# Optimization experiments

Hardware: AMD Instinct MI355X
Metric: run time of the kernel (lower is better)

Reference implementation:

```python
import jax, jax.numpy as jnp
import numpy as np

B, MAX_POINTS = 4, 100000
NPX, NPY, C = 512, 512, 64


def setup_inputs() -> dict:
    key = jax.random.key(0)
    k1, k2, k3, k4, k5, k6, k7 = jax.random.split(key, 7)
    grid_flow_embeddings = jax.random.normal(k1, (B, C, NPX, NPY), dtype=jnp.float32)
    point_cloud = jax.random.normal(k2, (B, MAX_POINTS, C), dtype=jnp.float32)
    # same pillar index replicated across the channel dim, as produced upstream
    pillar_idx = jax.random.randint(k3, (B, MAX_POINTS, 1), 0, NPX * NPY)
    indices = jnp.broadcast_to(pillar_idx, (B, MAX_POINTS, C)).astype(jnp.int64)
    # Linear(128, 32) and Linear(32, 3), torch layout: W [out, in], b [out]
    Y_w = jax.random.normal(k4, (32, 128), dtype=jnp.float32) / np.sqrt(128.0)
    Y_b = jax.random.normal(k5, (32,), dtype=jnp.float32) * 0.01
    Z_w = jax.random.normal(k6, (3, 32), dtype=jnp.float32) / np.sqrt(32.0)
    Z_b = jax.random.normal(k7, (3,), dtype=jnp.float32) * 0.01
    return {
        "grid_flow_embeddings": grid_flow_embeddings,
        "point_cloud": point_cloud,
        "indices": indices,
        "Y_w": Y_w,
        "Y_b": Y_b,
        "Z_w": Z_w,
        "Z_b": Z_b,
    }


def reference(grid_flow_embeddings, point_cloud, indices, Y_w, Y_b, Z_w, Z_b):
    b, c, nx, ny = grid_flow_embeddings.shape
    # permute (B,C,X,Y) -> (B,X,Y,C), flatten -> (B, X*Y, C)
    grid_flat = jnp.transpose(grid_flow_embeddings, (0, 2, 3, 1)).reshape(b, nx * ny, c)
    # gather along dim 1 with per-element indices (B, P, C)
    cell_embeddings = jnp.take_along_axis(grid_flat, indices, axis=1)
    full = jnp.concatenate([cell_embeddings, point_cloud], axis=2)  # (B, P, 128)
    full = jnp.einsum("bpf,of->bpo", full, Y_w) + Y_b                # (B, P, 32)
    full = jnp.einsum("bpf,of->bpo", full, Z_w) + Z_b                # (B, P, 3)
    return full
```

## Files before the change

### kernel.cpp

```cpp
#include <hip/hip_runtime.h>

#define BATCH 4
#define PTS   100000
#define CH    64
#define NPIX  (512 * 512)


#define WS_AG    0
#define WS_AP    1024
#define WS_BIAS  2048
#define WS_G3    4096

__global__ __launch_bounds__(128) void fold_weights_kernel(
    const float* __restrict__ Yw,
    const float* __restrict__ Yb,
    const float* __restrict__ Zw,
    const float* __restrict__ Zb,
    float* __restrict__ ws)
{
    const int f = threadIdx.x;
    float a0 = 0.f, a1 = 0.f, a2 = 0.f;
    for (int k = 0; k < 32; ++k) {
        const float y = Yw[k * 128 + f];
        a0 += Zw[0 * 32 + k] * y;
        a1 += Zw[1 * 32 + k] * y;
        a2 += Zw[2 * 32 + k] * y;
    }
    float4* dst = (f < 64) ? (float4*)((char*)ws + WS_AG) + f
                           : (float4*)((char*)ws + WS_AP) + (f - 64);
    *dst = make_float4(a0, a1, a2, 0.f);

    if (f == 0) {
        float b0 = Zb[0], b1 = Zb[1], b2 = Zb[2];
        for (int k = 0; k < 32; ++k) {
            const float y = Yb[k];
            b0 += Zw[0 * 32 + k] * y;
            b1 += Zw[1 * 32 + k] * y;
            b2 += Zw[2 * 32 + k] * y;
        }
        *(float4*)((char*)ws + WS_BIAS) = make_float4(b0, b1, b2, 0.f);
    }
}

__global__ __launch_bounds__(256) void grid_reduce_kernel(
    const float* __restrict__ grid,
    const float* __restrict__ ws_in,
    float* __restrict__ ws_out)
{
    __shared__ float4 sAg[64];
    if (threadIdx.x < 64)
        sAg[threadIdx.x] = ((const float4*)((const char*)ws_in + WS_AG))[threadIdx.x];
    __syncthreads();

    const int b = blockIdx.x >> 8;
    const int grp = ((blockIdx.x & 255) << 8) | threadIdx.x;
    const size_t pix0 = (size_t)grp * 4;

    const float* gbase = grid + (size_t)b * CH * NPIX + pix0;

    float4 acc0 = make_float4(0.f, 0.f, 0.f, 0.f);
    float4 acc1 = acc0;
    float4 acc2 = acc0;
#pragma unroll 8
    for (int c = 0; c < 64; ++c) {
        const float4 g = *(const float4*)(gbase + (size_t)c * NPIX);
        const float4 a = sAg[c];
        acc0.x += g.x * a.x; acc0.y += g.y * a.x; acc0.z += g.z * a.x; acc0.w += g.w * a.x;
        acc1.x += g.x * a.y; acc1.y += g.y * a.y; acc1.z += g.z * a.y; acc1.w += g.w * a.y;
        acc2.x += g.x * a.z; acc2.y += g.y * a.z; acc2.z += g.z * a.z; acc2.w += g.w * a.z;
    }

    float4* out4 = (float4*)((char*)ws_out + WS_G3) + ((size_t)b * NPIX + pix0);
    out4[0] = make_float4(acc0.x, acc1.x, acc2.x, 0.f);
    out4[1] = make_float4(acc0.y, acc1.y, acc2.y, 0.f);
    out4[2] = make_float4(acc0.z, acc1.z, acc2.z, 0.f);
    out4[3] = make_float4(acc0.w, acc1.w, acc2.w, 0.f);
}

__global__ __launch_bounds__(256) void point_kernel(
    const float* __restrict__ pc,
    const int*   __restrict__ idx,
    const float* __restrict__ ws,
    float* __restrict__ out)
{
    __shared__ float4 sAp[64];
    __shared__ float4 sBias;
    if (threadIdx.x < 64)
        sAp[threadIdx.x] = ((const float4*)((const char*)ws + WS_AP))[threadIdx.x];
    if (threadIdx.x == 64)
        sBias = *(const float4*)((const char*)ws + WS_BIAS);
    __syncthreads();

    const long long g = (long long)blockIdx.x * 256 + threadIdx.x;
    if (g >= (long long)BATCH * PTS) return;
    const int b = (int)(g / PTS);
    const int p = (int)(g % PTS);

    const int pillar = idx[((long long)b * PTS + p) * CH];
    const float4 gcell = ((const float4*)((const char*)ws + WS_G3))[(size_t)b * NPIX + pillar];

    float z0 = gcell.x + sBias.x;
    float z1 = gcell.y + sBias.y;
    float z2 = gcell.z + sBias.z;

    const float4* pb = (const float4*)(pc + ((size_t)b * PTS + p) * CH);
#pragma unroll
    for (int c4 = 0; c4 < 16; ++c4) {
        const float4 x = pb[c4];
        const float4 a0 = sAp[c4 * 4 + 0];
        const float4 a1 = sAp[c4 * 4 + 1];
        const float4 a2 = sAp[c4 * 4 + 2];
        const float4 a3 = sAp[c4 * 4 + 3];
        z0 += x.x * a0.x + x.y * a1.x + x.z * a2.x + x.w * a3.x;
        z1 += x.x * a0.y + x.y * a1.y + x.z * a2.y + x.w * a3.y;
        z2 += x.x * a0.z + x.y * a1.z + x.z * a2.z + x.w * a3.z;
    }

    float* op = out + g * 3;
    op[0] = z0;
    op[1] = z1;
    op[2] = z2;
}

extern "C" void kernel_launch(void* const* d_in, const int* in_sizes, int n_in,
                              void* d_out, int out_size, void* d_ws, size_t ws_size,
                              hipStream_t stream) {
    const float* grid = (const float*)d_in[0];
    const float* pc   = (const float*)d_in[1];
    const int*   idx  = (const int*)d_in[2];
    const float* Yw   = (const float*)d_in[3];
    const float* Yb   = (const float*)d_in[4];
    const float* Zw   = (const float*)d_in[5];
    const float* Zb   = (const float*)d_in[6];
    float* out = (float*)d_out;
    float* ws  = (float*)d_ws;

    hipLaunchKernelGGL(fold_weights_kernel, dim3(1), dim3(128), 0, stream,
                       Yw, Yb, Zw, Zb, ws);

    hipLaunchKernelGGL(grid_reduce_kernel, dim3(BATCH * 256), dim3(256), 0, stream,
                       grid, ws, ws);

    const int total = BATCH * PTS;
    const int blocks = (total + 255) / 256;
    hipLaunchKernelGGL(point_kernel, dim3(blocks), dim3(256), 0, stream,
                       pc, idx, ws, out);
}
```

Baseline: 499.6 us.

## Store reduced grid in bf16, fold weights per block, use nontemporal loads

Removes the separate weight-folding launch and recomputes the folded Linear weights inside each block of both kernels. The per-pixel reduced grid intermediate is now stored as bf16 (8 bytes per pixel instead of 16), which halves that write and the gather traffic. Streaming loads and stores use nontemporal hints. The bf16 intermediate adds rounding error to the output, and every block repeats the small weight fold.

```diff
diff --git a/kernel.cpp b/kernel.cpp
--- a/kernel.cpp
+++ b/kernel.cpp
@@ -6,50 +6,39 @@
 #define NPIX  (512 * 512)
 
 
-#define WS_AG    0
-#define WS_AP    1024
-#define WS_BIAS  2048
-#define WS_G3    4096
+typedef float  f32x4 __attribute__((ext_vector_type(4)));
+typedef unsigned int u32x4 __attribute__((ext_vector_type(4)));
 
-__global__ __launch_bounds__(128) void fold_weights_kernel(
-    const float* __restrict__ Yw,
-    const float* __restrict__ Yb,
-    const float* __restrict__ Zw,
-    const float* __restrict__ Zb,
-    float* __restrict__ ws)
-{
-    const int f = threadIdx.x;
-    float a0 = 0.f, a1 = 0.f, a2 = 0.f;
-    for (int k = 0; k < 32; ++k) {
-        const float y = Yw[k * 128 + f];
-        a0 += Zw[0 * 32 + k] * y;
-        a1 += Zw[1 * 32 + k] * y;
-        a2 += Zw[2 * 32 + k] * y;
-    }
-    float4* dst = (f < 64) ? (float4*)((char*)ws + WS_AG) + f
-                           : (float4*)((char*)ws + WS_AP) + (f - 64);
-    *dst = make_float4(a0, a1, a2, 0.f);
-
-    if (f == 0) {
-        float b0 = Zb[0], b1 = Zb[1], b2 = Zb[2];
-        for (int k = 0; k < 32; ++k) {
-            const float y = Yb[k];
-            b0 += Zw[0 * 32 + k] * y;
-            b1 += Zw[1 * 32 + k] * y;
-            b2 += Zw[2 * 32 + k] * y;
-        }
-        *(float4*)((char*)ws + WS_BIAS) = make_float4(b0, b1, b2, 0.f);
-    }
+__device__ inline unsigned short f2bf(float x) {
+    unsigned int u = __float_as_uint(x);
+    u += 0x7fffu + ((u >> 16) & 1u);
+    return (unsigned short)(u >> 16);
+}
+__device__ inline unsigned int pack2(float a, float b) {
+    return (unsigned int)f2bf(a) | ((unsigned int)f2bf(b) << 16);
+}
+__device__ inline float bf2f(unsigned short u) {
+    return __uint_as_float((unsigned int)u << 16);
 }
 
 __global__ __launch_bounds__(256) void grid_reduce_kernel(
     const float* __restrict__ grid,
-    const float* __restrict__ ws_in,
-    float* __restrict__ ws_out)
+    const float* __restrict__ Yw,
+    const float* __restrict__ Zw,
+    unsigned short* __restrict__ G3)
 {
-    __shared__ float4 sAg[64];
-    if (threadIdx.x < 64)
-        sAg[threadIdx.x] = ((const float4*)((const char*)ws_in + WS_AG))[threadIdx.x];
+    __shared__ f32x4 sAg[64];
+    if (threadIdx.x < 64) {
+        const int f = threadIdx.x;
+        float a0 = 0.f, a1 = 0.f, a2 = 0.f;
+        for (int k = 0; k < 32; ++k) {
+            const float y = Yw[k * 128 + f];
+            a0 += Zw[k] * y;
+            a1 += Zw[32 + k] * y;
+            a2 += Zw[64 + k] * y;
+        }
+        sAg[f] = (f32x4){a0, a1, a2, 0.f};
+    }
     __syncthreads();
 
     const int b = blockIdx.x >> 8;
@@ -58,37 +47,56 @@
 
     const float* gbase = grid + (size_t)b * CH * NPIX + pix0;
 
-    float4 acc0 = make_float4(0.f, 0.f, 0.f, 0.f);
-    float4 acc1 = acc0;
-    float4 acc2 = acc0;
+    f32x4 acc0 = (f32x4){0.f, 0.f, 0.f, 0.f};
+    f32x4 acc1 = acc0;
+    f32x4 acc2 = acc0;
 #pragma unroll 8
     for (int c = 0; c < 64; ++c) {
-        const float4 g = *(const float4*)(gbase + (size_t)c * NPIX);
-        const float4 a = sAg[c];
-        acc0.x += g.x * a.x; acc0.y += g.y * a.x; acc0.z += g.z * a.x; acc0.w += g.w * a.x;
-        acc1.x += g.x * a.y; acc1.y += g.y * a.y; acc1.z += g.z * a.y; acc1.w += g.w * a.y;
-        acc2.x += g.x * a.z; acc2.y += g.y * a.z; acc2.z += g.z * a.z; acc2.w += g.w * a.z;
+        const f32x4 g = __builtin_nontemporal_load((const f32x4*)(gbase + (size_t)c * NPIX));
+        const f32x4 a = sAg[c];
+        acc0 += g * a.x;
+        acc1 += g * a.y;
+        acc2 += g * a.z;
     }
 
-    float4* out4 = (float4*)((char*)ws_out + WS_G3) + ((size_t)b * NPIX + pix0);
-    out4[0] = make_float4(acc0.x, acc1.x, acc2.x, 0.f);
-    out4[1] = make_float4(acc0.y, acc1.y, acc2.y, 0.f);
-    out4[2] = make_float4(acc0.z, acc1.z, acc2.z, 0.f);
-    out4[3] = make_float4(acc0.w, acc1.w, acc2.w, 0.f);
+    u32x4 lo, hi;
+    lo.x = pack2(acc0.x, acc1.x); lo.y = pack2(acc2.x, 0.f);
+    lo.z = pack2(acc0.y, acc1.y); lo.w = pack2(acc2.y, 0.f);
+    hi.x = pack2(acc0.z, acc1.z); hi.y = pack2(acc2.z, 0.f);
+    hi.z = pack2(acc0.w, acc1.w); hi.w = pack2(acc2.w, 0.f);
+    u32x4* dst = (u32x4*)(G3 + ((size_t)b * NPIX + pix0) * 4);
+    dst[0] = lo;
+    dst[1] = hi;
 }
 
 __global__ __launch_bounds__(256) void point_kernel(
     const float* __restrict__ pc,
     const int*   __restrict__ idx,
-    const float* __restrict__ ws,
+    const float* __restrict__ Yw,
+    const float* __restrict__ Yb,
+    const float* __restrict__ Zw,
+    const float* __restrict__ Zb,
+    const unsigned short* __restrict__ G3,
     float* __restrict__ out)
 {
-    __shared__ float4 sAp[64];
-    __shared__ float4 sBias;
-    if (threadIdx.x < 64)
-        sAp[threadIdx.x] = ((const float4*)((const char*)ws + WS_AP))[threadIdx.x];
-    if (threadIdx.x == 64)
-        sBias = *(const float4*)((const char*)ws + WS_BIAS);
+    __shared__ f32x4 sAp[64];
+    __shared__ float sBias[3];
+    if (threadIdx.x < 64) {
+        const int f = 64 + threadIdx.x;
+        float a0 = 0.f, a1 = 0.f, a2 = 0.f;
+        for (int k = 0; k < 32; ++k) {
+            const float y = Yw[k * 128 + f];
+            a0 += Zw[k] * y;
+            a1 += Zw[32 + k] * y;
+            a2 += Zw[64 + k] * y;
+        }
+        sAp[threadIdx.x] = (f32x4){a0, a1, a2, 0.f};
+    } else if (threadIdx.x < 67) {
+        const int o = threadIdx.x - 64;
+        float s = Zb[o];
+        for (int k = 0; k < 32; ++k) s += Zw[o * 32 + k] * Yb[k];
+        sBias[o] = s;
+    }
     __syncthreads();
 
     const long long g = (long long)blockIdx.x * 256 + threadIdx.x;
@@ -96,30 +104,30 @@
     const int b = (int)(g / PTS);
     const int p = (int)(g % PTS);
 
-    const int pillar = idx[((long long)b * PTS + p) * CH];
-    const float4 gcell = ((const float4*)((const char*)ws + WS_G3))[(size_t)b * NPIX + pillar];
+    const int pillar = __builtin_nontemporal_load(idx + ((long long)b * PTS + p) * CH);
+    const ushort4 gc = *(const ushort4*)(G3 + ((size_t)b * NPIX + pillar) * 4);
 
-    float z0 = gcell.x + sBias.x;
-    float z1 = gcell.y + sBias.y;
-    float z2 = gcell.z + sBias.z;
+    float z0 = bf2f(gc.x) + sBias[0];
+    float z1 = bf2f(gc.y) + sBias[1];
+    float z2 = bf2f(gc.z) + sBias[2];
 
-    const float4* pb = (const float4*)(pc + ((size_t)b * PTS + p) * CH);
+    const float* pb = pc + ((size_t)b * PTS + p) * CH;
 #pragma unroll
     for (int c4 = 0; c4 < 16; ++c4) {
-        const float4 x = pb[c4];
-        const float4 a0 = sAp[c4 * 4 + 0];
-        const float4 a1 = sAp[c4 * 4 + 1];
-        const float4 a2 = sAp[c4 * 4 + 2];
-        const float4 a3 = sAp[c4 * 4 + 3];
+        const f32x4 x = __builtin_nontemporal_load((const f32x4*)(pb + c4 * 4));
+        const f32x4 a0 = sAp[c4 * 4 + 0];
+        const f32x4 a1 = sAp[c4 * 4 + 1];
+        const f32x4 a2 = sAp[c4 * 4 + 2];
+        const f32x4 a3 = sAp[c4 * 4 + 3];
         z0 += x.x * a0.x + x.y * a1.x + x.z * a2.x + x.w * a3.x;
         z1 += x.x * a0.y + x.y * a1.y + x.z * a2.y + x.w * a3.y;
         z2 += x.x * a0.z + x.y * a1.z + x.z * a2.z + x.w * a3.z;
     }
 
     float* op = out + g * 3;
-    op[0] = z0;
-    op[1] = z1;
-    op[2] = z2;
+    __builtin_nontemporal_store(z0, op + 0);
+    __builtin_nontemporal_store(z1, op + 1);
+    __builtin_nontemporal_store(z2, op + 2);
 }
 
 extern "C" void kernel_launch(void* const* d_in, const int* in_sizes, int n_in,
@@ -133,16 +141,13 @@
     const float* Zw   = (const float*)d_in[5];
     const float* Zb   = (const float*)d_in[6];
     float* out = (float*)d_out;
-    float* ws  = (float*)d_ws;
-
-    hipLaunchKernelGGL(fold_weights_kernel, dim3(1), dim3(128), 0, stream,
-                       Yw, Yb, Zw, Zb, ws);
+    unsigned short* G3 = (unsigned short*)d_ws;
 
     hipLaunchKernelGGL(grid_reduce_kernel, dim3(BATCH * 256), dim3(256), 0, stream,
-                       grid, ws, ws);
+                       grid, Yw, Zw, G3);
 
     const int total = BATCH * PTS;
     const int blocks = (total + 255) / 256;
     hipLaunchKernelGGL(point_kernel, dim3(blocks), dim3(256), 0, stream,
-                       pc, idx, ws, out);
+                       pc, idx, Yw, Yb, Zw, Zb, G3, out);
 }
```

Result: no change. 504.5 us (+1.0%).
